# Kernel optimization log

Measured on AMD Instinct MI355X. Metric: run time of the kernel, lower is better.

The kernel has to match this reference:

```python
import jax, jax.numpy as jnp
import numpy as np

N_NODES = 100000
N_EDGES = 3200000
OUT_DIM = 128


def setup_inputs() -> dict:
    key = jax.random.key(0)
    k1, k2, k3, k4, k5, k6 = jax.random.split(key, 6)
    return {
        "previous_inclusion_score": jax.random.normal(k1, (N_NODES,), dtype=jnp.float32),
        "nodes": jax.random.normal(k2, (N_NODES, 3), dtype=jnp.float32),
        "row_indices": jax.random.randint(k3, (N_EDGES,), 0, N_NODES, dtype=jnp.int32),
        "col_indices": jax.random.randint(k4, (N_EDGES,), 0, N_NODES, dtype=jnp.int32),
        "W_phi": jax.random.normal(k5, (OUT_DIM,), dtype=jnp.float32),
        "W_theta": jax.random.normal(k6, (3, 1), dtype=jnp.float32),
    }


def reference(previous_inclusion_score, nodes, row_indices, col_indices, W_phi, W_theta):
    # gather endpoints and project 3D differences through W_theta: [E,3] @ [3,1] -> [E,1]
    diff = nodes[row_indices] - nodes[col_indices]
    proj = diff @ W_theta
    # torch.norm over dim=1 of an [E,1] tensor == abs
    neigh_distances = jnp.abs(proj[:, 0])  # [E]
    # per-node max over incident edges; empty segments -> -inf, original leaves them 0
    max_distances = jax.ops.segment_max(neigh_distances, row_indices, num_segments=N_NODES)
    max_distances = jnp.maximum(max_distances, 0.0)  # distances are >= 0, so this matches the zeros default
    # outer product with W_phi: [N, D]
    list_inc_score = W_phi[None, :] * max_distances[:, None]
    # previous_inclusion_score is non-empty and D != 1 -> mean over feature dim, then average with previous
    inc_mean = jnp.mean(list_inc_score, axis=1)  # [N]
    return 0.5 * (previous_inclusion_score + inc_mean)
```

## Files before the change

kernel.cpp:

```cpp
#include <hip/hip_runtime.h>

#define OUT_DIM 128
#define CHUNK_LG 15
#define CHUNK (1 << CHUNK_LG)
#define PB 64
#define NT 1024

typedef int          vint4  __attribute__((ext_vector_type(4)));
typedef unsigned int vuint4 __attribute__((ext_vector_type(4)));
typedef unsigned int u32;

__device__ __forceinline__ u32 enc15(float d) {
    u32 b = __float_as_uint(d);
    b += 0x7FFFu + ((b >> 16) & 1u);
    return (b >> 16) & 0x7FFFu;
}

__global__ void init_kernel(float* __restrict__ p, float* __restrict__ meanW,
                            const float* __restrict__ nodes,
                            const float* __restrict__ Wt,
                            const float* __restrict__ W_phi, int n) {
    int i = blockIdx.x * blockDim.x + threadIdx.x;
    if (i < n) {
        float x = nodes[3 * i], y = nodes[3 * i + 1], z = nodes[3 * i + 2];
        p[i] = x * Wt[0] + y * Wt[1] + z * Wt[2];
    }
    if (blockIdx.x == 0 && threadIdx.x == 0) {
        float s = 0.0f;
        #pragma unroll
        for (int j = 0; j < OUT_DIM; ++j) s += W_phi[j];
        *meanW = s / (float)OUT_DIM;
    }
}

__global__ void encode_kernel(const float* __restrict__ p,
                              const int* __restrict__ row,
                              const int* __restrict__ col,
                              u32* __restrict__ key, int E) {
    int t = blockIdx.x * blockDim.x + threadIdx.x;
    int base = t * 4;
    if (base >= E) return;
    if (base + 3 < E) {
        vint4 r = __builtin_nontemporal_load((const vint4*)(row + base));
        vint4 c = __builtin_nontemporal_load((const vint4*)(col + base));
        float d0 = fabsf(p[r.x] - p[c.x]);
        float d1 = fabsf(p[r.y] - p[c.y]);
        float d2 = fabsf(p[r.z] - p[c.z]);
        float d3 = fabsf(p[r.w] - p[c.w]);
        vuint4 k;
        k.x = ((u32)r.x << 15) | enc15(d0);
        k.y = ((u32)r.y << 15) | enc15(d1);
        k.z = ((u32)r.z << 15) | enc15(d2);
        k.w = ((u32)r.w << 15) | enc15(d3);
        *(vuint4*)(key + base) = k;
    } else {
        for (int e = base; e < E; ++e)
            key[e] = ((u32)row[e] << 15) | enc15(fabsf(p[row[e]] - p[col[e]]));
    }
}

#define PROC(V) do { \
        if ((V.x >> (15 + CHUNK_LG)) == uc) atomicMax(&lds[(V.x >> 15) & (CHUNK - 1)], V.x & 0x7FFFu); \
        if ((V.y >> (15 + CHUNK_LG)) == uc) atomicMax(&lds[(V.y >> 15) & (CHUNK - 1)], V.y & 0x7FFFu); \
        if ((V.z >> (15 + CHUNK_LG)) == uc) atomicMax(&lds[(V.z >> 15) & (CHUNK - 1)], V.z & 0x7FFFu); \
        if ((V.w >> (15 + CHUNK_LG)) == uc) atomicMax(&lds[(V.w >> 15) & (CHUNK - 1)], V.w & 0x7FFFu); \
    } while (0)

__global__ __launch_bounds__(NT) void chunkmax_kernel(const u32* __restrict__ key,
                                                      u32* __restrict__ partial,
                                                      int E, int nch) {
    __shared__ u32 lds[CHUNK];
    int c = blockIdx.x / PB;
    int b = blockIdx.x % PB;
    vuint4 zero = {0u, 0u, 0u, 0u};
    vuint4* lds4 = (vuint4*)lds;
    for (int i = threadIdx.x; i < CHUNK / 4; i += NT) lds4[i] = zero;
    __syncthreads();

    int G = E >> 2;
    int per = (G + PB - 1) / PB;
    int s = b * per;
    int e = min(s + per, G);
    const vuint4* key4 = (const vuint4*)key;
    u32 uc = (u32)c;
    const int step = NT;
    int k = s + (int)threadIdx.x;
    for (; k + 3 * step < e; k += 4 * step) {
        vuint4 a0 = key4[k];
        vuint4 a1 = key4[k + step];
        vuint4 a2 = key4[k + 2 * step];
        vuint4 a3 = key4[k + 3 * step];
        PROC(a0); PROC(a1); PROC(a2); PROC(a3);
    }
    for (; k < e; k += step) {
        vuint4 a0 = key4[k];
        PROC(a0);
    }
    if (b == PB - 1) {
        for (int j = (G << 2) + (int)threadIdx.x; j < E; j += step) {
            u32 v = key[j];
            if ((v >> (15 + CHUNK_LG)) == uc) atomicMax(&lds[(v >> 15) & (CHUNK - 1)], v & 0x7FFFu);
        }
    }
    __syncthreads();
    u32* dst = partial + ((size_t)c * PB + b) * (CHUNK / 2);
    for (int j = threadIdx.x; j < CHUNK / 2; j += NT)
        dst[j] = lds[2 * j] | (lds[2 * j + 1] << 16);
}

__global__ void reduce_final_kernel(const float* __restrict__ prev,
                                    const u32* __restrict__ partial,
                                    const float* __restrict__ meanW,
                                    float* __restrict__ out, int n) {
    int t = blockIdx.x * blockDim.x + threadIdx.x;
    int i0 = t * 2;
    if (i0 >= n) return;
    int chunk = i0 >> CHUNK_LG;
    int local = i0 & (CHUNK - 1);
    const u32* base = partial + (size_t)chunk * PB * (CHUNK / 2) + (local >> 1);
    u32 mlo = 0, mhi = 0;
    #pragma unroll
    for (int b = 0; b < PB; ++b) {
        u32 v = base[(size_t)b * (CHUNK / 2)];
        mlo = max(mlo, v & 0xFFFFu);
        mhi = max(mhi, v >> 16);
    }
    float mw = *meanW;
    float flo = __uint_as_float(mlo << 16);
    float fhi = __uint_as_float(mhi << 16);
    out[i0] = 0.5f * (prev[i0] + mw * flo);
    if (i0 + 1 < n)
        out[i0 + 1] = 0.5f * (prev[i0 + 1] + mw * fhi);
}

__global__ void fb_zero_kernel(float* __restrict__ maxd, float* __restrict__ p,
                               float* __restrict__ meanW,
                               const float* __restrict__ nodes,
                               const float* __restrict__ Wt,
                               const float* __restrict__ W_phi, int n) {
    int i = blockIdx.x * blockDim.x + threadIdx.x;
    if (i < n) {
        maxd[i] = 0.0f;
        float x = nodes[3 * i], y = nodes[3 * i + 1], z = nodes[3 * i + 2];
        p[i] = x * Wt[0] + y * Wt[1] + z * Wt[2];
    }
    if (blockIdx.x == 0 && threadIdx.x == 0) {
        float s = 0.0f;
        for (int j = 0; j < OUT_DIM; ++j) s += W_phi[j];
        *meanW = s / (float)OUT_DIM;
    }
}
__global__ void fb_edge_kernel(const float* __restrict__ p,
                               const int* __restrict__ row,
                               const int* __restrict__ col,
                               float* __restrict__ maxd, int E) {
    int t = blockIdx.x * blockDim.x + threadIdx.x;
    int base = t * 4;
    if (base >= E) return;
    if (base + 3 < E) {
        vint4 r = __builtin_nontemporal_load((const vint4*)(row + base));
        vint4 c = __builtin_nontemporal_load((const vint4*)(col + base));
        atomicMax((int*)&maxd[r.x], __float_as_int(fabsf(p[r.x] - p[c.x])));
        atomicMax((int*)&maxd[r.y], __float_as_int(fabsf(p[r.y] - p[c.y])));
        atomicMax((int*)&maxd[r.z], __float_as_int(fabsf(p[r.z] - p[c.z])));
        atomicMax((int*)&maxd[r.w], __float_as_int(fabsf(p[r.w] - p[c.w])));
    } else {
        for (int e = base; e < E; ++e) {
            float d = fabsf(p[row[e]] - p[col[e]]);
            atomicMax((int*)&maxd[row[e]], __float_as_int(d));
        }
    }
}
__global__ void fb_final_kernel(const float* __restrict__ prev,
                                const float* __restrict__ maxd,
                                const float* __restrict__ meanW,
                                float* __restrict__ out, int n) {
    int i = blockIdx.x * blockDim.x + threadIdx.x;
    if (i < n) out[i] = 0.5f * (prev[i] + (*meanW) * maxd[i]);
}

extern "C" void kernel_launch(void* const* d_in, const int* in_sizes, int n_in,
                              void* d_out, int out_size, void* d_ws, size_t ws_size,
                              hipStream_t stream) {
    const float* prev    = (const float*)d_in[0];
    const float* nodes   = (const float*)d_in[1];
    const int*   row     = (const int*)d_in[2];
    const int*   col     = (const int*)d_in[3];
    const float* W_phi   = (const float*)d_in[4];
    const float* W_theta = (const float*)d_in[5];

    const int N = in_sizes[0];
    const int E = in_sizes[2];
    float* out = (float*)d_out;
    const int B = 256;

    const int nch = (N + CHUNK - 1) >> CHUNK_LG;

    size_t pBytes    = ((size_t)N * 4 + 15) & ~(size_t)15;
    size_t keyBytes  = (((size_t)E + 3) & ~(size_t)3) * 4;
    size_t partBytes = (size_t)nch * PB * (CHUNK / 2) * 4;
    size_t need = pBytes + keyBytes + partBytes + 4;

    if (ws_size >= need && N <= (1 << 17)) {
        float* p     = (float*)d_ws;
        u32*   key   = (u32*)((char*)d_ws + pBytes);
        u32*   part  = (u32*)((char*)d_ws + pBytes + keyBytes);
        float* meanW = (float*)((char*)d_ws + pBytes + keyBytes + partBytes);

        init_kernel<<<(N + B - 1) / B, B, 0, stream>>>(p, meanW, nodes, W_theta, W_phi, N);
        int tE = (E + 3) / 4;
        encode_kernel<<<(tE + B - 1) / B, B, 0, stream>>>(p, row, col, key, E);
        chunkmax_kernel<<<nch * PB, NT, 0, stream>>>(key, part, E, nch);
        int tN = (N + 1) / 2;
        reduce_final_kernel<<<(tN + B - 1) / B, B, 0, stream>>>(prev, part, meanW, out, N);
    } else {
        float* p     = (float*)d_ws;
        float* maxd  = (float*)d_ws + N;
        float* meanW = (float*)d_ws + 2 * (size_t)N;
        fb_zero_kernel<<<(N + B - 1) / B, B, 0, stream>>>(maxd, p, meanW, nodes, W_theta, W_phi, N);
        int tE = (E + 3) / 4;
        fb_edge_kernel<<<(tE + B - 1) / B, B, 0, stream>>>(p, row, col, maxd, E);
        fb_final_kernel<<<(N + B - 1) / B, B, 0, stream>>>(prev, maxd, meanW, out, N);
    }
}
```

Before: 55.10 us.

## Fuse four pipeline kernels into one persistent kernel with grid barriers

Replaces the init, encode, chunk-max and reduce kernels with a single persistent kernel of 256 blocks of 1024 threads that steps through the phases using atomic-counter global barriers, plus a tiny setup kernel that zeroes the counters and computes the W_phi mean. This removes the launch gaps and tail drain between the kernels. In exchange, the encode phase runs on only 256 blocks rather than a fully oversubscribed grid, which may cut latency hiding for the random gathers. The barriers also assume all 256 blocks are co-resident, and the N limit drops to 4 chunks.

New measurement: 140.1 us. 2.54x slower.

```diff
diff --git a/kernel.cpp b/kernel.cpp
--- a/kernel.cpp
+++ b/kernel.cpp
@@ -5,6 +5,7 @@
 #define CHUNK (1 << CHUNK_LG)
 #define PB 64
 #define NT 1024
+#define GRID 256
 
 typedef int          vint4  __attribute__((ext_vector_type(4)));
 typedef unsigned int vuint4 __attribute__((ext_vector_type(4)));
@@ -16,46 +17,24 @@
     return (b >> 16) & 0x7FFFu;
 }
 
-__global__ void init_kernel(float* __restrict__ p, float* __restrict__ meanW,
-                            const float* __restrict__ nodes,
-                            const float* __restrict__ Wt,
-                            const float* __restrict__ W_phi, int n) {
-    int i = blockIdx.x * blockDim.x + threadIdx.x;
-    if (i < n) {
-        float x = nodes[3 * i], y = nodes[3 * i + 1], z = nodes[3 * i + 2];
-        p[i] = x * Wt[0] + y * Wt[1] + z * Wt[2];
-    }
-    if (blockIdx.x == 0 && threadIdx.x == 0) {
+__device__ __forceinline__ void gbar(u32* c, u32 nb) {
+    __syncthreads();
+    if (threadIdx.x == 0) {
+        __hip_atomic_fetch_add(c, 1u, __ATOMIC_RELEASE, __HIP_MEMORY_SCOPE_AGENT);
+        while (__hip_atomic_load(c, __ATOMIC_ACQUIRE, __HIP_MEMORY_SCOPE_AGENT) < nb)
+            __builtin_amdgcn_s_sleep(1);
+    }
+    __syncthreads();
+}
+
+__global__ void setup_kernel(u32* __restrict__ cnt, float* __restrict__ meanW,
+                             const float* __restrict__ W_phi) {
+    if (threadIdx.x < 8) cnt[threadIdx.x] = 0;
+    if (threadIdx.x == 0) {
         float s = 0.0f;
         #pragma unroll
         for (int j = 0; j < OUT_DIM; ++j) s += W_phi[j];
         *meanW = s / (float)OUT_DIM;
-    }
-}
-
-__global__ void encode_kernel(const float* __restrict__ p,
-                              const int* __restrict__ row,
-                              const int* __restrict__ col,
-                              u32* __restrict__ key, int E) {
-    int t = blockIdx.x * blockDim.x + threadIdx.x;
-    int base = t * 4;
-    if (base >= E) return;
-    if (base + 3 < E) {
-        vint4 r = __builtin_nontemporal_load((const vint4*)(row + base));
-        vint4 c = __builtin_nontemporal_load((const vint4*)(col + base));
-        float d0 = fabsf(p[r.x] - p[c.x]);
-        float d1 = fabsf(p[r.y] - p[c.y]);
-        float d2 = fabsf(p[r.z] - p[c.z]);
-        float d3 = fabsf(p[r.w] - p[c.w]);
-        vuint4 k;
-        k.x = ((u32)r.x << 15) | enc15(d0);
-        k.y = ((u32)r.y << 15) | enc15(d1);
-        k.z = ((u32)r.z << 15) | enc15(d2);
-        k.w = ((u32)r.w << 15) | enc15(d3);
-        *(vuint4*)(key + base) = k;
-    } else {
-        for (int e = base; e < E; ++e)
-            key[e] = ((u32)row[e] << 15) | enc15(fabsf(p[row[e]] - p[col[e]]));
     }
 }
 
@@ -66,71 +45,112 @@
         if ((V.w >> (15 + CHUNK_LG)) == uc) atomicMax(&lds[(V.w >> 15) & (CHUNK - 1)], V.w & 0x7FFFu); \
     } while (0)
 
-__global__ __launch_bounds__(NT) void chunkmax_kernel(const u32* __restrict__ key,
-                                                      u32* __restrict__ partial,
-                                                      int E, int nch) {
+__global__ __launch_bounds__(NT) void fused_kernel(
+        const float* __restrict__ prev, const float* __restrict__ nodes,
+        const int* __restrict__ row, const int* __restrict__ col,
+        const float* __restrict__ Wt, const float* __restrict__ meanW,
+        float* __restrict__ p, u32* __restrict__ key, u32* __restrict__ partial,
+        u32* __restrict__ cnt, float* __restrict__ out, int N, int E, int nch) {
     __shared__ u32 lds[CHUNK];
-    int c = blockIdx.x / PB;
-    int b = blockIdx.x % PB;
-    vuint4 zero = {0u, 0u, 0u, 0u};
-    vuint4* lds4 = (vuint4*)lds;
-    for (int i = threadIdx.x; i < CHUNK / 4; i += NT) lds4[i] = zero;
-    __syncthreads();
-
-    int G = E >> 2;
-    int per = (G + PB - 1) / PB;
-    int s = b * per;
-    int e = min(s + per, G);
-    const vuint4* key4 = (const vuint4*)key;
-    u32 uc = (u32)c;
-    const int step = NT;
-    int k = s + (int)threadIdx.x;
-    for (; k + 3 * step < e; k += 4 * step) {
-        vuint4 a0 = key4[k];
-        vuint4 a1 = key4[k + step];
-        vuint4 a2 = key4[k + 2 * step];
-        vuint4 a3 = key4[k + 3 * step];
-        PROC(a0); PROC(a1); PROC(a2); PROC(a3);
-    }
-    for (; k < e; k += step) {
-        vuint4 a0 = key4[k];
-        PROC(a0);
-    }
-    if (b == PB - 1) {
-        for (int j = (G << 2) + (int)threadIdx.x; j < E; j += step) {
-            u32 v = key[j];
-            if ((v >> (15 + CHUNK_LG)) == uc) atomicMax(&lds[(v >> 15) & (CHUNK - 1)], v & 0x7FFFu);
-        }
-    }
-    __syncthreads();
-    u32* dst = partial + ((size_t)c * PB + b) * (CHUNK / 2);
-    for (int j = threadIdx.x; j < CHUNK / 2; j += NT)
-        dst[j] = lds[2 * j] | (lds[2 * j + 1] << 16);
-}
-
-__global__ void reduce_final_kernel(const float* __restrict__ prev,
-                                    const u32* __restrict__ partial,
-                                    const float* __restrict__ meanW,
-                                    float* __restrict__ out, int n) {
-    int t = blockIdx.x * blockDim.x + threadIdx.x;
-    int i0 = t * 2;
-    if (i0 >= n) return;
-    int chunk = i0 >> CHUNK_LG;
-    int local = i0 & (CHUNK - 1);
-    const u32* base = partial + (size_t)chunk * PB * (CHUNK / 2) + (local >> 1);
-    u32 mlo = 0, mhi = 0;
-    #pragma unroll
-    for (int b = 0; b < PB; ++b) {
-        u32 v = base[(size_t)b * (CHUNK / 2)];
-        mlo = max(mlo, v & 0xFFFFu);
-        mhi = max(mhi, v >> 16);
-    }
-    float mw = *meanW;
-    float flo = __uint_as_float(mlo << 16);
-    float fhi = __uint_as_float(mhi << 16);
-    out[i0] = 0.5f * (prev[i0] + mw * flo);
-    if (i0 + 1 < n)
-        out[i0 + 1] = 0.5f * (prev[i0 + 1] + mw * fhi);
+    int bid = blockIdx.x;
+    int tid = threadIdx.x;
+
+    {
+        int i = bid * NT + tid;
+        if (i < N) {
+            float x = nodes[3 * i], y = nodes[3 * i + 1], z = nodes[3 * i + 2];
+            p[i] = x * Wt[0] + y * Wt[1] + z * Wt[2];
+        }
+    }
+    gbar(&cnt[0], GRID);
+
+    {
+        int G = E >> 2;
+        int per = (G + GRID - 1) / GRID;
+        int s = bid * per;
+        int e = min(s + per, G);
+        const vint4* row4 = (const vint4*)row;
+        const vint4* col4 = (const vint4*)col;
+        for (int g = s + tid; g < e; g += NT) {
+            vint4 r = __builtin_nontemporal_load(row4 + g);
+            vint4 c = __builtin_nontemporal_load(col4 + g);
+            vuint4 k;
+            k.x = ((u32)r.x << 15) | enc15(fabsf(p[r.x] - p[c.x]));
+            k.y = ((u32)r.y << 15) | enc15(fabsf(p[r.y] - p[c.y]));
+            k.z = ((u32)r.z << 15) | enc15(fabsf(p[r.z] - p[c.z]));
+            k.w = ((u32)r.w << 15) | enc15(fabsf(p[r.w] - p[c.w]));
+            *(vuint4*)(key + 4 * g) = k;
+        }
+        if (bid == GRID - 1) {
+            for (int j = (G << 2) + tid; j < E; j += NT)
+                key[j] = ((u32)row[j] << 15) | enc15(fabsf(p[row[j]] - p[col[j]]));
+        }
+    }
+    gbar(&cnt[1], GRID);
+
+    {
+        int c = bid / PB;
+        int b = bid % PB;
+        if (c < nch) {
+            vuint4 zero = {0u, 0u, 0u, 0u};
+            vuint4* lds4 = (vuint4*)lds;
+            for (int i = tid; i < CHUNK / 4; i += NT) lds4[i] = zero;
+            __syncthreads();
+
+            int G = E >> 2;
+            int per = (G + PB - 1) / PB;
+            int s = b * per;
+            int e = min(s + per, G);
+            const vuint4* key4 = (const vuint4*)key;
+            u32 uc = (u32)c;
+            const int step = NT;
+            int k = s + tid;
+            for (; k + 3 * step < e; k += 4 * step) {
+                vuint4 a0 = key4[k];
+                vuint4 a1 = key4[k + step];
+                vuint4 a2 = key4[k + 2 * step];
+                vuint4 a3 = key4[k + 3 * step];
+                PROC(a0); PROC(a1); PROC(a2); PROC(a3);
+            }
+            for (; k < e; k += step) {
+                vuint4 a0 = key4[k];
+                PROC(a0);
+            }
+            if (b == PB - 1) {
+                for (int j = (G << 2) + tid; j < E; j += step) {
+                    u32 v = key[j];
+                    if ((v >> (15 + CHUNK_LG)) == uc)
+                        atomicMax(&lds[(v >> 15) & (CHUNK - 1)], v & 0x7FFFu);
+                }
+            }
+            __syncthreads();
+            u32* dst = partial + ((size_t)c * PB + b) * (CHUNK / 2);
+            for (int j = tid; j < CHUNK / 2; j += NT)
+                dst[j] = lds[2 * j] | (lds[2 * j + 1] << 16);
+        }
+    }
+    gbar(&cnt[2], GRID);
+
+    {
+        int t = bid * NT + tid;
+        int i0 = t * 2;
+        if (i0 < N) {
+            int chunk = i0 >> CHUNK_LG;
+            int local = i0 & (CHUNK - 1);
+            const u32* base = partial + (size_t)chunk * PB * (CHUNK / 2) + (local >> 1);
+            u32 mlo = 0, mhi = 0;
+            #pragma unroll
+            for (int b = 0; b < PB; ++b) {
+                u32 v = base[(size_t)b * (CHUNK / 2)];
+                mlo = max(mlo, v & 0xFFFFu);
+                mhi = max(mhi, v >> 16);
+            }
+            float mw = *meanW;
+            out[i0] = 0.5f * (prev[i0] + mw * __uint_as_float(mlo << 16));
+            if (i0 + 1 < N)
+                out[i0 + 1] = 0.5f * (prev[i0 + 1] + mw * __uint_as_float(mhi << 16));
+        }
+    }
 }
 
 __global__ void fb_zero_kernel(float* __restrict__ maxd, float* __restrict__ p,
@@ -196,23 +216,21 @@
 
     const int nch = (N + CHUNK - 1) >> CHUNK_LG;
 
-    size_t pBytes    = ((size_t)N * 4 + 15) & ~(size_t)15;
-    size_t keyBytes  = (((size_t)E + 3) & ~(size_t)3) * 4;
-    size_t partBytes = (size_t)nch * PB * (CHUNK / 2) * 4;
-    size_t need = pBytes + keyBytes + partBytes + 4;
-
-    if (ws_size >= need && N <= (1 << 17)) {
+    size_t pBytes    = ((size_t)N * 4 + 255) & ~(size_t)255;
+    size_t keyBytes  = ((((size_t)E + 3) & ~(size_t)3) * 4 + 255) & ~(size_t)255;
+    size_t partBytes = (size_t)4 * PB * (CHUNK / 2) * 4;
+    size_t need = pBytes + keyBytes + partBytes + 8 * 4 + 4;
+
+    if (ws_size >= need && N <= 4 * CHUNK) {
         float* p     = (float*)d_ws;
         u32*   key   = (u32*)((char*)d_ws + pBytes);
         u32*   part  = (u32*)((char*)d_ws + pBytes + keyBytes);
-        float* meanW = (float*)((char*)d_ws + pBytes + keyBytes + partBytes);
-
-        init_kernel<<<(N + B - 1) / B, B, 0, stream>>>(p, meanW, nodes, W_theta, W_phi, N);
-        int tE = (E + 3) / 4;
-        encode_kernel<<<(tE + B - 1) / B, B, 0, stream>>>(p, row, col, key, E);
-        chunkmax_kernel<<<nch * PB, NT, 0, stream>>>(key, part, E, nch);
-        int tN = (N + 1) / 2;
-        reduce_final_kernel<<<(tN + B - 1) / B, B, 0, stream>>>(prev, part, meanW, out, N);
+        u32*   cnt   = (u32*)((char*)d_ws + pBytes + keyBytes + partBytes);
+        float* meanW = (float*)((char*)d_ws + pBytes + keyBytes + partBytes + 8 * 4);
+
+        setup_kernel<<<1, 64, 0, stream>>>(cnt, meanW, W_phi);
+        fused_kernel<<<GRID, NT, 0, stream>>>(prev, nodes, row, col, W_theta,
+                                              meanW, p, key, part, cnt, out, N, E, nch);
     } else {
         float* p     = (float*)d_ws;
         float* maxd  = (float*)d_ws + N;
```
